# Performance work log

Hardware: AMD Instinct MI355X
Metric: run time of the kernel (lower is better)

The kernel has to match this reference:

```python
import jax, jax.numpy as jnp
import numpy as np

INPUT_DIM = 1024
TAGSET = 16
EMBED = 1024
HIDDEN = 2048
INTERM = 1024
T = 4096
START_IDX = 0  # y_codebook['__START__']


def setup_inputs() -> dict:
    key = jax.random.key(0)
    ks = jax.random.split(key, 11)
    def w(k, shape, fan_in):
        return (jax.random.normal(k, shape, jnp.float32) / np.sqrt(fan_in)).astype(jnp.float32)
    cat = INPUT_DIM + TAGSET  # x_t concatenated with one-hot of previous tag
    return {
        "seq": jax.random.normal(ks[0], (1, T, INPUT_DIM), jnp.float32),
        "W_embed": w(ks[1], (EMBED, cat), cat),
        "b_embed": jnp.zeros((EMBED,), jnp.float32),
        "W_ih": w(ks[2], (4 * HIDDEN, EMBED), EMBED),
        "W_hh": w(ks[3], (4 * HIDDEN, HIDDEN), HIDDEN),
        "b_ih": jnp.zeros((4 * HIDDEN,), jnp.float32),
        "b_hh": jnp.zeros((4 * HIDDEN,), jnp.float32),
        "W_interm": w(ks[4], (INTERM, HIDDEN), HIDDEN),
        "b_interm": jnp.zeros((INTERM,), jnp.float32),
        "W_tag": w(ks[5], (TAGSET, INTERM), INTERM),
        "b_tag": jnp.zeros((TAGSET,), jnp.float32),
    }


def _forward(seq, W_embed, b_embed, W_ih, W_hh, b_ih, b_hh, W_interm, b_interm, W_tag, b_tag):
    def step(carry, x_t):
        h, c, prev_oh = carry
        xin = jnp.concatenate([x_t, prev_oh])              # [INPUT_DIM+TAGSET]
        e = jax.nn.relu(W_embed @ xin + b_embed)           # embed + nonlinearity
        gates = W_ih @ e + b_ih + W_hh @ h + b_hh          # [4H], torch gate order i,f,g,o
        i, f, g, o = jnp.split(gates, 4)
        c = jax.nn.sigmoid(f) * c + jax.nn.sigmoid(i) * jnp.tanh(g)
        h = jax.nn.sigmoid(o) * jnp.tanh(c)
        inter = jax.nn.relu(W_interm @ h + b_interm)
        tag_space = W_tag @ inter + b_tag                  # [TAGSET]
        logp = jax.nn.log_softmax(tag_space)
        prob = jax.nn.softmax(tag_space)
        pred = jnp.argmax(logp)
        new_oh = jax.lax.stop_gradient(jax.nn.one_hot(pred, TAGSET, dtype=seq.dtype))
        return (h, c, new_oh), (logp, prob, pred)

    h0 = jnp.zeros((HIDDEN,), seq.dtype)
    c0 = jnp.zeros((HIDDEN,), seq.dtype)
    oh0 = jax.nn.one_hot(START_IDX, TAGSET, dtype=seq.dtype)
    _, (logps, probs, preds) = jax.lax.scan(step, (h0, c0, oh0), seq[0])
    return logps, probs, preds.astype(jnp.int32)


def reference(seq, W_embed, b_embed, W_ih, W_hh, b_ih, b_hh, W_interm, b_interm, W_tag, b_tag):
    return _forward(seq, W_embed, b_embed, W_ih, W_hh, b_ih, b_hh, W_interm, b_interm, W_tag, b_tag)
```

## Files before the change

### kernel.cpp

```cpp
#include <hip/hip_runtime.h>
#include <math.h>

#define T_STEPS 4096
#define EMB 1024
#define HID 2048
#define CAT 1040
#define TAG 16
#define NBLK 256
#define NTHR 1024
#define FLAG_STRIDE 32

#define OUT_LOGP 0
#define OUT_PROB (T_STEPS * TAG)
#define OUT_PRED (2 * T_STEPS * TAG)

__device__ __forceinline__ float sigf(float x) { return 1.0f / (1.0f + expf(-x)); }

__device__ __forceinline__ unsigned aloadu(const unsigned* p) {
  return __hip_atomic_load(p, __ATOMIC_RELAXED, __HIP_MEMORY_SCOPE_AGENT);
}
__device__ __forceinline__ void astoreu(unsigned* p, unsigned v) {
  __hip_atomic_store(p, v, __ATOMIC_RELAXED, __HIP_MEMORY_SCOPE_AGENT);
}
__device__ __forceinline__ float aloadf(const float* p) {
  return __hip_atomic_load(p, __ATOMIC_RELAXED, __HIP_MEMORY_SCOPE_AGENT);
}
__device__ __forceinline__ void astoref(float* p, float v) {
  __hip_atomic_store(p, v, __ATOMIC_RELAXED, __HIP_MEMORY_SCOPE_AGENT);
}

__global__ __launch_bounds__(256) void rnnss_vt_kernel(const float* __restrict__ We,
                                                       float* __restrict__ VT) {
  int n = blockIdx.x * 256 + threadIdx.x;
  int p = n >> 10, i = n & 1023;
  VT[n] = We[(size_t)i * CAT + EMB + p];
}

__global__ __launch_bounds__(256) void rnnss_uprep(const float* __restrict__ X,
                                                   const float* __restrict__ W,
                                                   const float* __restrict__ be,
                                                   float* __restrict__ U) {
  __shared__ __align__(16) float As[32][68];
  __shared__ __align__(16) float Bs[32][68];
  const int bm = blockIdx.x * 64;
  const int bn = blockIdx.y * 64;
  const int tid = threadIdx.x;
  const int tx = tid & 15, ty = tid >> 4;
  const int lr = tid >> 5, lc = tid & 31;
  float acc[4][4] = {};
  for (int k0 = 0; k0 < EMB; k0 += 32) {
#pragma unroll
    for (int p = 0; p < 8; ++p) {
      As[lc][lr + 8 * p] = X[(size_t)(bm + lr + 8 * p) * EMB + k0 + lc];
      Bs[lc][lr + 8 * p] = W[(size_t)(bn + lr + 8 * p) * CAT + k0 + lc];
    }
    __syncthreads();
#pragma unroll 8
    for (int k = 0; k < 32; ++k) {
      const float4 a = *(const float4*)&As[k][ty * 4];
      const float4 v = *(const float4*)&Bs[k][tx * 4];
      float am[4] = {a.x, a.y, a.z, a.w};
      float bv[4] = {v.x, v.y, v.z, v.w};
#pragma unroll
      for (int m = 0; m < 4; ++m)
#pragma unroll
        for (int n = 0; n < 4; ++n) acc[m][n] = fmaf(am[m], bv[n], acc[m][n]);
    }
    __syncthreads();
  }
#pragma unroll
  for (int m = 0; m < 4; ++m)
#pragma unroll
    for (int n = 0; n < 4; ++n)
      U[(size_t)(bm + ty * 4 + m) * EMB + bn + tx * 4 + n] =
          acc[m][n] + be[bn + tx * 4 + n];
}

__global__ __launch_bounds__(NTHR, 4) void rnnss_persist(
    const float* __restrict__ Wih, const float* __restrict__ Whh,
    const float* __restrict__ bih, const float* __restrict__ bhh,
    const float* __restrict__ Witm, const float* __restrict__ bitm,
    const float* __restrict__ Wtag, const float* __restrict__ btag,
    const float* __restrict__ U, const float* __restrict__ VT,
    float* __restrict__ hbase,
    float* __restrict__ tpg,
    unsigned* __restrict__ flags,
    float* __restrict__ out) {
  __shared__ __align__(16) float sWi[32 * 1024];
  __shared__ __align__(16) float se[EMB];
  __shared__ __align__(16) float sh[HID];
  __shared__ float sacc1[NTHR];
  __shared__ float sg[32];
  __shared__ float wpart[16];
  __shared__ float stv[TAG];
  __shared__ float sc[8];

  const int tid = threadIdx.x;
  const int b = blockIdx.x;
  const int u0 = b * 8;
  if (tid < 8) sc[tid] = 0.0f;
  sh[tid] = 0.0f;
  sh[tid + 1024] = 0.0f;
  sacc1[tid] = 0.0f;

  const int rt = tid >> 5;
  const int q = tid & 31;
  const int gsec = rt >> 3, j = rt & 7;
  const int grow = gsec * HID + u0 + j;
  const float bsum = bih[grow] + bhh[grow];
  const float4* __restrict__ wh = (const float4*)(Whh + (size_t)grow * HID);

  const int brow = tid >> 8, bq = tid & 255;
  const float4* __restrict__ wm = (const float4*)(Witm + (size_t)(b * 4 + brow) * HID);
  float bi0 = 0, bi1 = 0, bi2 = 0, bi3 = 0;
  float wt0 = 0, wt1 = 0, wt2 = 0, wt3 = 0;
  if (tid < TAG) {
    bi0 = bitm[b * 4 + 0];
    bi1 = bitm[b * 4 + 1];
    bi2 = bitm[b * 4 + 2];
    bi3 = bitm[b * 4 + 3];
    wt0 = Wtag[(size_t)tid * 1024 + b * 4 + 0];
    wt1 = Wtag[(size_t)tid * 1024 + b * 4 + 1];
    wt2 = Wtag[(size_t)tid * 1024 + b * 4 + 2];
    wt3 = Wtag[(size_t)tid * 1024 + b * 4 + 3];
  }
  float btw = 0.0f;
  if ((tid & 63) == 0) btw = btag[tid >> 6];

  {
    const float4* WiF = (const float4*)Wih;
    float4* sWiF = (float4*)sWi;
#pragma unroll
    for (int n = 0; n < 8; ++n) {
      int idx = tid + 1024 * n;
      int r = idx >> 8, c = idx & 255;
      int gr = (r >> 3) * HID + u0 + (r & 7);
      sWiF[idx] = WiF[(size_t)gr * 256 + c];
    }
  }

  float4 rwh[16], rwm[2];
#pragma unroll
  for (int it = 0; it < 16; ++it) rwh[it] = wh[q + 32 * it];
  rwm[0] = wm[bq];
  rwm[1] = wm[bq + 256];
#pragma unroll
  for (int it = 0; it < 16; ++it)
    asm volatile("" : "+v"(rwh[it].x), "+v"(rwh[it].y), "+v"(rwh[it].z), "+v"(rwh[it].w));
  asm volatile("" : "+v"(rwm[0].x), "+v"(rwm[0].y), "+v"(rwm[0].z), "+v"(rwm[0].w));
  asm volatile("" : "+v"(rwm[1].x), "+v"(rwm[1].y), "+v"(rwm[1].z), "+v"(rwm[1].w));

  const float4* sef = (const float4*)se;
  const float4* shf = (const float4*)sh;
  const float4* sWiF4 = (const float4*)sWi;

  int pred = 0;
  float u_cur = U[tid];
  __syncthreads();

  for (int t = 0; t < T_STEPS; ++t) {
    float* __restrict__ hrow = hbase + (size_t)t * HID;
    const unsigned epA = 2u * (unsigned)t + 1u;

    {
      float ev = u_cur + VT[(size_t)pred * EMB + tid];
      se[tid] = ev > 0.0f ? ev : 0.0f;
    }
    __syncthreads();
    float acc0 = 0.0f;
#pragma unroll
    for (int it = 0; it < 8; ++it) {
      float4 w = sWiF4[rt * 256 + q + 32 * it], x = sef[q + 32 * it];
      acc0 += w.x * x.x + w.y * x.y + w.z * x.z + w.w * x.w;
    }
    float acc = acc0 + sacc1[tid];
#pragma unroll
    for (int d = 16; d > 0; d >>= 1) acc += __shfl_down(acc, d, 32);
    if (q == 0) sg[rt] = acc + bsum;
    __syncthreads();
    if (tid < 8) {
      float iv = sigf(sg[tid]);
      float fv = sigf(sg[8 + tid]);
      float gv = tanhf(sg[16 + tid]);
      float ov = sigf(sg[24 + tid]);
      float c = fv * sc[tid] + iv * gv;
      sc[tid] = c;
      astoref(hrow + u0 + tid, ov * tanhf(c));
    }
    if (tid == 0) {
      asm volatile("s_waitcnt vmcnt(0)" ::: "memory");
      astoreu(flags + (size_t)b * FLAG_STRIDE, epA);
    }
    if (tid < NBLK) {
      const unsigned* f = flags + (size_t)tid * FLAG_STRIDE;
      while (aloadu(f) < epA) __builtin_amdgcn_s_sleep(1);
    }
    asm volatile("" ::: "memory");
    __syncthreads();

    if (tid < 512) ((float4*)sh)[tid] = ((const float4*)hrow)[tid];
    float u_nxt = (t + 1 < T_STEPS) ? U[(size_t)(t + 1) * EMB + tid] : 0.0f;
    __syncthreads();

    {
      float a2 = 0.0f;
      float4 w = rwm[0], x = shf[bq];
      a2 += w.x * x.x + w.y * x.y + w.z * x.z + w.w * x.w;
      w = rwm[1]; x = shf[bq + 256];
      a2 += w.x * x.x + w.y * x.y + w.z * x.z + w.w * x.w;
#pragma unroll
      for (int d = 32; d > 0; d >>= 1) a2 += __shfl_down(a2, d, 64);
      if ((tid & 63) == 0) wpart[tid >> 6] = a2;
    }
    __syncthreads();
    if (tid < TAG) {
      float i0 = wpart[0] + wpart[1] + wpart[2] + wpart[3] + bi0;
      float i1 = wpart[4] + wpart[5] + wpart[6] + wpart[7] + bi1;
      float i2 = wpart[8] + wpart[9] + wpart[10] + wpart[11] + bi2;
      float i3 = wpart[12] + wpart[13] + wpart[14] + wpart[15] + bi3;
      i0 = i0 > 0.0f ? i0 : 0.0f;
      i1 = i1 > 0.0f ? i1 : 0.0f;
      i2 = i2 > 0.0f ? i2 : 0.0f;
      i3 = i3 > 0.0f ? i3 : 0.0f;
      astoref(tpg + tid * NBLK + b, wt0 * i0 + wt1 * i1 + wt2 * i2 + wt3 * i3);
    }
    if (tid == 0) {
      asm volatile("s_waitcnt vmcnt(0)" ::: "memory");
      astoreu(flags + (size_t)b * FLAG_STRIDE, epA + 1u);
    }

    {
      float a1 = 0.0f;
#pragma unroll
      for (int it = 0; it < 16; ++it) {
        float4 w = rwh[it], x = shf[q + 32 * it];
        a1 += w.x * x.x + w.y * x.y + w.z * x.z + w.w * x.w;
      }
      sacc1[tid] = a1;
    }

    if (tid < NBLK) {
      const unsigned* f = flags + (size_t)tid * FLAG_STRIDE;
      while (aloadu(f) < epA + 1u) __builtin_amdgcn_s_sleep(1);
    }
    asm volatile("" ::: "memory");
    __syncthreads();

    {
      const int w = tid >> 6, l = tid & 63;
      float v = aloadf(tpg + w * NBLK + l) + aloadf(tpg + w * NBLK + 64 + l) +
                aloadf(tpg + w * NBLK + 128 + l) + aloadf(tpg + w * NBLK + 192 + l);
#pragma unroll
      for (int d = 32; d > 0; d >>= 1) v += __shfl_down(v, d, 64);
      if (l == 0) stv[w] = v + btw;
    }
    __syncthreads();
    {
      int am = 0;
      float bv = stv[0];
#pragma unroll
      for (int k = 1; k < TAG; ++k) {
        if (stv[k] > bv) { bv = stv[k]; am = k; }
      }
      pred = am;
      if (b == 0) {
        if (tid < TAG) {
          float m = stv[0];
#pragma unroll
          for (int k = 1; k < TAG; ++k) m = fmaxf(m, stv[k]);
          float s = expf(stv[tid] - m);
#pragma unroll
          for (int msk = 8; msk > 0; msk >>= 1) s += __shfl_xor(s, msk, 16);
          float ls = logf(s);
          float lp = stv[tid] - m - ls;
          out[OUT_LOGP + t * TAG + tid] = lp;
          out[OUT_PROB + t * TAG + tid] = expf(lp);
        } else if (tid == TAG) {
          out[OUT_PRED + t] = (float)am;
        }
      }
      u_cur = u_nxt;
    }
  }
}

extern "C" void kernel_launch(void* const* d_in, const int* in_sizes, int n_in,
                              void* d_out, int out_size, void* d_ws, size_t ws_size,
                              hipStream_t stream) {
  const float* seq = (const float*)d_in[0];
  const float* W_embed = (const float*)d_in[1];
  const float* b_embed = (const float*)d_in[2];
  const float* W_ih = (const float*)d_in[3];
  const float* W_hh = (const float*)d_in[4];
  const float* b_ih = (const float*)d_in[5];
  const float* b_hh = (const float*)d_in[6];
  const float* W_interm = (const float*)d_in[7];
  const float* b_interm = (const float*)d_in[8];
  const float* W_tag = (const float*)d_in[9];
  const float* b_tag = (const float*)d_in[10];
  (void)in_sizes; (void)n_in; (void)out_size; (void)ws_size;

  const size_t flg_b = (size_t)NBLK * FLAG_STRIDE * 4;
  const size_t tp_b = (size_t)TAG * NBLK * 4;
  const size_t vt_b = (size_t)TAG * EMB * 4;
  const size_t h_b = (size_t)T_STEPS * HID * 4;

  char* ws = (char*)d_ws;
  unsigned* flags = (unsigned*)ws;
  float* tpg = (float*)(ws + flg_b);
  float* VT = (float*)(ws + flg_b + tp_b);
  float* hbase = (float*)(ws + flg_b + tp_b + vt_b);
  float* U = (float*)(ws + flg_b + tp_b + vt_b + h_b);
  float* out = (float*)d_out;

  hipMemsetAsync(ws, 0, flg_b, stream);

  hipLaunchKernelGGL(rnnss_vt_kernel, dim3((TAG * EMB) / 256), dim3(256), 0, stream,
                     W_embed, VT);
  hipLaunchKernelGGL(rnnss_uprep, dim3(T_STEPS / 64, EMB / 64), dim3(256), 0, stream,
                     seq, W_embed, b_embed, U);

  void* args[] = {
      (void*)&W_ih,    (void*)&W_hh,  (void*)&b_ih,  (void*)&b_hh,
      (void*)&W_interm,(void*)&b_interm, (void*)&W_tag, (void*)&b_tag,
      (void*)&U,       (void*)&VT,    (void*)&hbase, (void*)&tpg,
      (void*)&flags,   (void*)&out};
  hipLaunchCooperativeKernel((const void*)rnnss_persist, dim3(NBLK), dim3(NTHR),
                             args, 0, stream);
}
```

Measured before the change: 33.59 ms.

## Replace first grid barrier with epoch-tagged 64-bit hidden-state payloads

Each block now writes its hidden units as 64-bit words that pack the step epoch with the value. Consumers spin on the exact words they need instead of waiting on all 256 block flags and then reading h. This removes one full grid barrier per step and drops the per-step h history buffer in favour of a single reused buffer. The risk is a WAR hazard: a block could overwrite h for step t+1 before a slow block has read step t. The remaining barrier likely prevents that, since every block reads h before it signals the second flag.

```diff
diff --git a/kernel.cpp b/kernel.cpp
--- a/kernel.cpp
+++ b/kernel.cpp
@@ -27,6 +27,21 @@
 }
 __device__ __forceinline__ void astoref(float* p, float v) {
   __hip_atomic_store(p, v, __ATOMIC_RELAXED, __HIP_MEMORY_SCOPE_AGENT);
+}
+__device__ __forceinline__ unsigned long long aload64(const unsigned long long* p) {
+  return __hip_atomic_load(p, __ATOMIC_RELAXED, __HIP_MEMORY_SCOPE_AGENT);
+}
+__device__ __forceinline__ void astore64(unsigned long long* p, unsigned long long v) {
+  __hip_atomic_store(p, v, __ATOMIC_RELAXED, __HIP_MEMORY_SCOPE_AGENT);
+}
+__device__ __forceinline__ unsigned long long pack(unsigned ep, float v) {
+  return ((unsigned long long)ep << 32) | (unsigned long long)__float_as_uint(v);
+}
+__device__ __forceinline__ float val32(unsigned long long v) {
+  return __uint_as_float((unsigned)v);
+}
+__device__ __forceinline__ int epok(unsigned long long v, unsigned ep) {
+  return (unsigned)(v >> 32) == ep;
 }
 
 __global__ __launch_bounds__(256) void rnnss_vt_kernel(const float* __restrict__ We,
@@ -82,7 +97,7 @@
     const float* __restrict__ Witm, const float* __restrict__ bitm,
     const float* __restrict__ Wtag, const float* __restrict__ btag,
     const float* __restrict__ U, const float* __restrict__ VT,
-    float* __restrict__ hbase,
+    unsigned long long* __restrict__ hpay,
     float* __restrict__ tpg,
     unsigned* __restrict__ flags,
     float* __restrict__ out) {
@@ -159,8 +174,7 @@
   __syncthreads();
 
   for (int t = 0; t < T_STEPS; ++t) {
-    float* __restrict__ hrow = hbase + (size_t)t * HID;
-    const unsigned epA = 2u * (unsigned)t + 1u;
+    const unsigned ep = (unsigned)t + 1u;
 
     {
       float ev = u_cur + VT[(size_t)pred * EMB + tid];
@@ -185,20 +199,20 @@
       float ov = sigf(sg[24 + tid]);
       float c = fv * sc[tid] + iv * gv;
       sc[tid] = c;
-      astoref(hrow + u0 + tid, ov * tanhf(c));
-    }
-    if (tid == 0) {
-      asm volatile("s_waitcnt vmcnt(0)" ::: "memory");
-      astoreu(flags + (size_t)b * FLAG_STRIDE, epA);
-    }
-    if (tid < NBLK) {
-      const unsigned* f = flags + (size_t)tid * FLAG_STRIDE;
-      while (aloadu(f) < epA) __builtin_amdgcn_s_sleep(1);
-    }
-    asm volatile("" ::: "memory");
-    __syncthreads();
-
-    if (tid < 512) ((float4*)sh)[tid] = ((const float4*)hrow)[tid];
+      astore64(hpay + u0 + tid, pack(ep, ov * tanhf(c)));
+    }
+
+    {
+      const int lane = tid & 63;
+      const int base = (tid >> 6) * 128 + lane;
+      const unsigned long long* hp = hpay + base;
+      unsigned long long v0 = aload64(hp);
+      unsigned long long v1 = aload64(hp + 64);
+      while (!epok(v0, ep)) { __builtin_amdgcn_s_sleep(1); v0 = aload64(hp); }
+      while (!epok(v1, ep)) { __builtin_amdgcn_s_sleep(1); v1 = aload64(hp + 64); }
+      sh[base] = val32(v0);
+      sh[base + 64] = val32(v1);
+    }
     float u_nxt = (t + 1 < T_STEPS) ? U[(size_t)(t + 1) * EMB + tid] : 0.0f;
     __syncthreads();
 
@@ -226,7 +240,7 @@
     }
     if (tid == 0) {
       asm volatile("s_waitcnt vmcnt(0)" ::: "memory");
-      astoreu(flags + (size_t)b * FLAG_STRIDE, epA + 1u);
+      astoreu(flags + (size_t)b * FLAG_STRIDE, ep);
     }
 
     {
@@ -241,7 +255,7 @@
 
     if (tid < NBLK) {
       const unsigned* f = flags + (size_t)tid * FLAG_STRIDE;
-      while (aloadu(f) < epA + 1u) __builtin_amdgcn_s_sleep(1);
+      while (aloadu(f) < ep) __builtin_amdgcn_s_sleep(1);
     }
     asm volatile("" ::: "memory");
     __syncthreads();
@@ -301,19 +315,19 @@
   (void)in_sizes; (void)n_in; (void)out_size; (void)ws_size;
 
   const size_t flg_b = (size_t)NBLK * FLAG_STRIDE * 4;
+  const size_t hp_b = (size_t)HID * 8;
   const size_t tp_b = (size_t)TAG * NBLK * 4;
   const size_t vt_b = (size_t)TAG * EMB * 4;
-  const size_t h_b = (size_t)T_STEPS * HID * 4;
 
   char* ws = (char*)d_ws;
   unsigned* flags = (unsigned*)ws;
-  float* tpg = (float*)(ws + flg_b);
-  float* VT = (float*)(ws + flg_b + tp_b);
-  float* hbase = (float*)(ws + flg_b + tp_b + vt_b);
-  float* U = (float*)(ws + flg_b + tp_b + vt_b + h_b);
+  unsigned long long* hpay = (unsigned long long*)(ws + flg_b);
+  float* tpg = (float*)(ws + flg_b + hp_b);
+  float* VT = (float*)(ws + flg_b + hp_b + tp_b);
+  float* U = (float*)(ws + flg_b + hp_b + tp_b + vt_b);
   float* out = (float*)d_out;
 
-  hipMemsetAsync(ws, 0, flg_b, stream);
+  hipMemsetAsync(ws, 0, flg_b + hp_b, stream);
 
   hipLaunchKernelGGL(rnnss_vt_kernel, dim3((TAG * EMB) / 256), dim3(256), 0, stream,
                      W_embed, VT);
@@ -323,7 +337,7 @@
   void* args[] = {
       (void*)&W_ih,    (void*)&W_hh,  (void*)&b_ih,  (void*)&b_hh,
       (void*)&W_interm,(void*)&b_interm, (void*)&W_tag, (void*)&b_tag,
-      (void*)&U,       (void*)&VT,    (void*)&hbase, (void*)&tpg,
+      (void*)&U,       (void*)&VT,    (void*)&hpay,  (void*)&tpg,
       (void*)&flags,   (void*)&out};
   hipLaunchCooperativeKernel((const void*)rnnss_persist, dim3(NBLK), dim3(NTHR),
                              args, 0, stream);
```

Result: no change. 33.19 ms (-1.2%).
